# Performance work log

Measured on AMD Instinct MI355X. Metric: run time of the kernel, lower is better.

Reference implementation:

```python
import jax, jax.numpy as jnp
import numpy as np

B, S, I, H = 16, 2048, 1024, 1024


def setup_inputs() -> dict:
    key = jax.random.key(0)
    ks = jax.random.split(key, 12)
    sc = 0.03  # small init so tanh/sigmoid are not saturated
    return {
        "x": jax.random.normal(ks[0], (B, S, I), dtype=jnp.float32),
        "attn_w1": sc * jax.random.normal(ks[1], (H, I), dtype=jnp.float32),
        "attn_b1": sc * jax.random.normal(ks[2], (H,), dtype=jnp.float32),
        "attn_w2": sc * jax.random.normal(ks[3], (1, H), dtype=jnp.float32),
        "attn_b2": sc * jax.random.normal(ks[4], (1,), dtype=jnp.float32),
        "w_ih": sc * jax.random.normal(ks[5], (3 * H, I), dtype=jnp.float32),
        "w_hh": sc * jax.random.normal(ks[6], (3 * H, H), dtype=jnp.float32),
        "b_ih": sc * jax.random.normal(ks[7], (3 * H,), dtype=jnp.float32),
        "b_hh": sc * jax.random.normal(ks[8], (3 * H,), dtype=jnp.float32),
        "fc_w": sc * jax.random.normal(ks[9], (I, H), dtype=jnp.float32),
        "fc_b": sc * jax.random.normal(ks[10], (I,), dtype=jnp.float32),
    }


def reference(x, attn_w1, attn_b1, attn_w2, attn_b2, w_ih, w_hh, b_ih, b_hh, fc_w, fc_b):
    b, s, i = x.shape
    h_dim = w_hh.shape[1]
    # Attention: per-timestep Linear-Tanh-Linear-Softmax, vectorized over time.
    ha = jnp.tanh(jnp.einsum('bsi,hi->bsh', x, attn_w1) + attn_b1)
    scores = jnp.einsum('bsh,oh->bso', ha, attn_w2) + attn_b2  # [B,S,1]
    # torch applies Softmax(dim=1) on [B,1] per timestep -> softmax over size-1 axis
    attn = jax.nn.softmax(scores, axis=2)  # [B,S,1] (identically ones)
    x_w = x * attn
    # GRU (1 layer): precompute input projections over all timesteps.
    gi = jnp.einsum('bsi,gi->bsg', x_w, w_ih) + b_ih  # [B,S,3H]

    def step(h, gi_t):
        gh = h @ w_hh.T + b_hh
        i_r, i_z, i_n = jnp.split(gi_t, 3, axis=-1)
        h_r, h_z, h_n = jnp.split(gh, 3, axis=-1)
        r = jax.nn.sigmoid(i_r + h_r)
        z = jax.nn.sigmoid(i_z + h_z)
        n = jnp.tanh(i_n + r * h_n)
        h_new = (1.0 - z) * n + z * h
        return h_new, h_new

    h0 = jnp.zeros((b, h_dim), dtype=x.dtype)
    h_last, outs = jax.lax.scan(step, h0, jnp.swapaxes(gi, 0, 1))  # outs: [S,B,H]
    rnn_out = jnp.swapaxes(outs, 0, 1)  # [B,S,H]
    output = jnp.einsum('bsh,ih->bsi', rnn_out, fc_w) + fc_b
    hidden = h_last[None]  # [num_layers=1, B, H]
    return (output, hidden, attn)
```

## Files before the change

kernel.cpp:

```cpp
#include <hip/hip_runtime.h>

typedef __attribute__((ext_vector_type(8))) short bh8;
typedef __attribute__((ext_vector_type(4))) float f32x4;

#define BATCH 16
#define SEQ 2048
#define M_ROWS (BATCH * SEQ)
#define KDIM 1024

__device__ __forceinline__ unsigned short f2bf(float f) {
  unsigned u = __float_as_uint(f);
  u = (u + 0x7FFFu + ((u >> 16) & 1u)) >> 16;
  return (unsigned short)u;
}
__device__ __forceinline__ float bf2f(unsigned short h) {
  return __uint_as_float(((unsigned)h) << 16);
}

__device__ __forceinline__ f32x4 mfma_bf16(bh8 a, bh8 b, f32x4 c) {
  return __builtin_amdgcn_mfma_f32_16x16x32_bf16(a, b, c, 0, 0, 0);
}

__device__ __forceinline__ void gl2lds16(const void* g, void* l) {
  __builtin_amdgcn_global_load_lds(
      (const __attribute__((address_space(1))) void*)g,
      (__attribute__((address_space(3))) void*)l, 16, 0, 0);
}

__global__ void cvt_bf16_kernel(const float* __restrict__ in,
                                unsigned short* __restrict__ out, int n4) {
  int i = blockIdx.x * blockDim.x + threadIdx.x;
  if (i >= n4) return;
  float4 v = ((const float4*)in)[i];
  ushort4 o;
  o.x = f2bf(v.x); o.y = f2bf(v.y); o.z = f2bf(v.z); o.w = f2bf(v.w);
  ((ushort4*)out)[i] = o;
}

__global__ void fill_ones_kernel(float* __restrict__ p, int n) {
  int i = blockIdx.x * blockDim.x + threadIdx.x;
  if (i < n) p[i] = 1.0f;
}

template<bool BF16OUT>
__global__ __launch_bounds__(256, 2) void gemm_nt(
    const unsigned short* __restrict__ A,
    const unsigned short* __restrict__ Bm,
    void* __restrict__ Cout,
    const float* __restrict__ bias,
    int N)
{
  __shared__ unsigned short As[128 * 32];
  __shared__ unsigned short Bs[128 * 32];
  const int tid = threadIdx.x;
  const int wave = tid >> 6, lane = tid & 63;
  const long tileM = (long)blockIdx.y * 128;
  const long tileN = (long)blockIdx.x * 128;

  const int srow = wave * 16 + (lane >> 2);
  const int scol = (lane & 3) * 8;
  const unsigned short* ga = A + (tileM + srow) * KDIM + scol;
  const unsigned short* gb = Bm + (tileN + srow) * KDIM + scol;
  unsigned short* la = As + wave * 512;
  unsigned short* lb = Bs + wave * 512;

  f32x4 acc[4][4];
  #pragma unroll
  for (int i = 0; i < 4; ++i)
    #pragma unroll
    for (int j = 0; j < 4; ++j)
      acc[i][j] = (f32x4){0.f, 0.f, 0.f, 0.f};

  const int wm = wave >> 1, wn = wave & 1;
  const int q = lane >> 4, mr = lane & 15;

  #pragma unroll 1
  for (int kt = 0; kt < 32; ++kt) {
    const int ko = kt * 32;
    gl2lds16(ga + ko, la);
    gl2lds16(ga + (long)64 * KDIM + ko, la + 2048);
    gl2lds16(gb + ko, lb);
    gl2lds16(gb + (long)64 * KDIM + ko, lb + 2048);
    __syncthreads();

    bh8 af[4], bfv[4];
    #pragma unroll
    for (int t = 0; t < 4; ++t)
      af[t] = *(const bh8*)&As[(wm * 64 + t * 16 + mr) * 32 + q * 8];
    #pragma unroll
    for (int t = 0; t < 4; ++t)
      bfv[t] = *(const bh8*)&Bs[(wn * 64 + t * 16 + mr) * 32 + q * 8];

    #pragma unroll
    for (int mt = 0; mt < 4; ++mt)
      #pragma unroll
      for (int nt = 0; nt < 4; ++nt)
        acc[mt][nt] = mfma_bf16(af[mt], bfv[nt], acc[mt][nt]);
    __syncthreads();
  }

  #pragma unroll
  for (int mt = 0; mt < 4; ++mt) {
    #pragma unroll
    for (int nt = 0; nt < 4; ++nt) {
      long n = tileN + wn * 64 + nt * 16 + mr;
      #pragma unroll
      for (int i = 0; i < 4; ++i) {
        long m = tileM + wm * 64 + mt * 16 + q * 4 + i;
        if constexpr (BF16OUT) {
          ((unsigned short*)Cout)[m * N + n] = f2bf(acc[mt][nt][i]);
        } else {
          ((float*)Cout)[m * N + n] = acc[mt][nt][i] + bias[n];
        }
      }
    }
  }
}

#define GRU_WGS 64
__global__ __launch_bounds__(256, 1) void gru_kernel(
    const unsigned short* __restrict__ gi,
    const unsigned short* __restrict__ whh,
    const float* __restrict__ b_ih,
    const float* __restrict__ b_hh,
    unsigned short* __restrict__ hbuf,
    unsigned short* __restrict__ rnn,
    float* __restrict__ hidden_out,
    unsigned* __restrict__ ctr)
{
  const int wg = blockIdx.x;
  const int tid = threadIdx.x;
  const int wv = tid >> 6, lane = tid & 63;
  const int D0 = wg * 16;
  const int q = lane >> 4, nn = lane & 15;

  bh8 wf[3][8];
  #pragma unroll
  for (int g = 0; g < 3; ++g)
    #pragma unroll
    for (int kk = 0; kk < 8; ++kk) {
      int k = wv * 256 + kk * 32 + q * 8;
      wf[g][kk] = *(const bh8*)&whh[(size_t)(g * 1024 + D0 + nn) * 1024 + k];
    }

  const int b = tid >> 4, dd = tid & 15, d = D0 + dd;
  const float bir = b_ih[d], biz = b_ih[1024 + d], bin_ = b_ih[2048 + d];
  const float bhr = b_hh[d], bhz = b_hh[1024 + d], bhn = b_hh[2048 + d];
  float hreg = 0.0f;
  const unsigned short* gi_base = gi + (size_t)b * SEQ * 3072 + d;

  __shared__ float red[4][3][16][16];

  #pragma unroll 1
  for (int s = 0; s < SEQ; ++s) {
    const unsigned short* hsrc = hbuf + (s & 1) * 16384;
    unsigned short* hdst = hbuf + ((s + 1) & 1) * 16384;

    f32x4 acc0 = {0.f,0.f,0.f,0.f}, acc1 = {0.f,0.f,0.f,0.f}, acc2 = {0.f,0.f,0.f,0.f};
    #pragma unroll
    for (int kk = 0; kk < 8; ++kk) {
      int k = wv * 256 + kk * 32 + q * 8;
      bh8 af = *(const bh8*)&hsrc[nn * 1024 + k];
      acc0 = mfma_bf16(af, wf[0][kk], acc0);
      acc1 = mfma_bf16(af, wf[1][kk], acc1);
      acc2 = mfma_bf16(af, wf[2][kk], acc2);
    }
    #pragma unroll
    for (int i = 0; i < 4; ++i) {
      red[wv][0][q * 4 + i][nn] = acc0[i];
      red[wv][1][q * 4 + i][nn] = acc1[i];
      red[wv][2][q * 4 + i][nn] = acc2[i];
    }
    __syncthreads();

    float ghr = red[0][0][b][dd] + red[1][0][b][dd] + red[2][0][b][dd] + red[3][0][b][dd];
    float ghz = red[0][1][b][dd] + red[1][1][b][dd] + red[2][1][b][dd] + red[3][1][b][dd];
    float ghn = red[0][2][b][dd] + red[1][2][b][dd] + red[2][2][b][dd] + red[3][2][b][dd];

    const unsigned short* gr = gi_base + (size_t)s * 3072;
    float gir = bf2f(gr[0]);
    float giz = bf2f(gr[1024]);
    float gin = bf2f(gr[2048]);

    float xr = gir + bir + ghr + bhr;
    float xz = giz + biz + ghz + bhz;
    float r = 1.0f / (1.0f + __expf(-xr));
    float z = 1.0f / (1.0f + __expf(-xz));
    float u = gin + bin_ + r * (ghn + bhn);
    float e = __expf(-2.0f * fabsf(u));
    float t = (1.0f - e) / (1.0f + e);
    float nv = copysignf(t, u);
    hreg = (1.0f - z) * nv + z * hreg;

    unsigned short hb = f2bf(hreg);
    hdst[b * 1024 + d] = hb;
    rnn[((size_t)b * SEQ + s) * 1024 + d] = hb;
    if (s == SEQ - 1) hidden_out[b * 1024 + d] = hreg;

    __syncthreads();
    if (tid == 0) {
      __hip_atomic_fetch_add(&ctr[s], 1u, __ATOMIC_RELEASE, __HIP_MEMORY_SCOPE_AGENT);
      unsigned v;
      do {
        v = __hip_atomic_load(&ctr[s], __ATOMIC_RELAXED, __HIP_MEMORY_SCOPE_AGENT);
      } while (v < (unsigned)GRU_WGS);
      (void)__hip_atomic_load(&ctr[s], __ATOMIC_ACQUIRE, __HIP_MEMORY_SCOPE_AGENT);
    }
    __syncthreads();
  }
}

extern "C" void kernel_launch(void* const* d_in, const int* in_sizes, int n_in,
                              void* d_out, int out_size, void* d_ws, size_t ws_size,
                              hipStream_t stream) {
  const float* x    = (const float*)d_in[0];
  const float* w_ih = (const float*)d_in[5];
  const float* w_hh = (const float*)d_in[6];
  const float* b_ih = (const float*)d_in[7];
  const float* b_hh = (const float*)d_in[8];
  const float* fc_w = (const float*)d_in[9];
  const float* fc_b = (const float*)d_in[10];

  float* out        = (float*)d_out;
  float* hidden_out = out + (size_t)M_ROWS * 1024;
  float* attn_out   = hidden_out + 16 * 1024;

  char* ws = (char*)d_ws;
  unsigned short* x_bf   = (unsigned short*)(ws);
  unsigned short* wih_bf = (unsigned short*)(ws + 67108864);
  unsigned short* whh_bf = (unsigned short*)(ws + 73400320);
  unsigned short* fcw_bf = (unsigned short*)(ws + 79691776);
  unsigned short* gi_bf  = (unsigned short*)(ws + 81788928);
  unsigned short* rnn_bf = (unsigned short*)(ws + 283115520);
  unsigned short* hbuf   = (unsigned short*)(ws + 350224384);
  unsigned*       ctr    = (unsigned*)(ws + 350289920);

  hipMemsetAsync(hbuf, 0, 65536 + 8192, stream);

  cvt_bf16_kernel<<<32768, 256, 0, stream>>>(x, x_bf, 8388608);
  cvt_bf16_kernel<<<3072, 256, 0, stream>>>(w_ih, wih_bf, 786432);
  cvt_bf16_kernel<<<3072, 256, 0, stream>>>(w_hh, whh_bf, 786432);
  cvt_bf16_kernel<<<1024, 256, 0, stream>>>(fc_w, fcw_bf, 262144);
  fill_ones_kernel<<<128, 256, 0, stream>>>(attn_out, 32768);

  gemm_nt<true><<<dim3(24, 256), 256, 0, stream>>>(x_bf, wih_bf, gi_bf, nullptr, 3072);

  gru_kernel<<<GRU_WGS, 256, 0, stream>>>(gi_bf, whh_bf, b_ih, b_hh, hbuf, rnn_bf,
                                          hidden_out, ctr);

  gemm_nt<false><<<dim3(8, 256), 256, 0, stream>>>(rnn_bf, fcw_bf, out, fc_b, 1024);
}
```

Baseline: 13.39 ms.

## Replace GRU grid barrier with step-tagged hidden-state words and polled loads

```diff
diff --git a/kernel.cpp b/kernel.cpp
--- a/kernel.cpp
+++ b/kernel.cpp
@@ -42,7 +42,7 @@
   if (i < n) p[i] = 1.0f;
 }
 
-template<bool BF16OUT>
+template<int MODE>
 __global__ __launch_bounds__(256, 2) void gemm_nt(
     const unsigned short* __restrict__ A,
     const unsigned short* __restrict__ Bm,
@@ -107,10 +107,13 @@
       #pragma unroll
       for (int i = 0; i < 4; ++i) {
         long m = tileM + wm * 64 + mt * 16 + q * 4 + i;
-        if constexpr (BF16OUT) {
-          ((unsigned short*)Cout)[m * N + n] = f2bf(acc[mt][nt][i]);
+        if constexpr (MODE == 0) {
+          ((float*)Cout)[m * N + n] = acc[mt][nt][i] + bias[n];
         } else {
-          ((float*)Cout)[m * N + n] = acc[mt][nt][i] + bias[n];
+          int b = (int)(m >> 11), s = (int)(m & 2047);
+          int g = (int)(n >> 10), wgi = (int)((n >> 4) & 63), dd = (int)(n & 15);
+          size_t idx = ((size_t)s * 64 + wgi) * 768 + (size_t)g * 256 + b * 16 + dd;
+          ((unsigned short*)Cout)[idx] = f2bf(acc[mt][nt][i]);
         }
       }
     }
@@ -123,10 +126,9 @@
     const unsigned short* __restrict__ whh,
     const float* __restrict__ b_ih,
     const float* __restrict__ b_hh,
-    unsigned short* __restrict__ hbuf,
+    unsigned* __restrict__ hdw,
     unsigned short* __restrict__ rnn,
-    float* __restrict__ hidden_out,
-    unsigned* __restrict__ ctr)
+    float* __restrict__ hidden_out)
 {
   const int wg = blockIdx.x;
   const int tid = threadIdx.x;
@@ -147,23 +149,43 @@
   const float bir = b_ih[d], biz = b_ih[1024 + d], bin_ = b_ih[2048 + d];
   const float bhr = b_hh[d], bhz = b_hh[1024 + d], bhn = b_hh[2048 + d];
   float hreg = 0.0f;
-  const unsigned short* gi_base = gi + (size_t)b * SEQ * 3072 + d;
 
   __shared__ float red[4][3][16][16];
 
   #pragma unroll 1
   for (int s = 0; s < SEQ; ++s) {
-    const unsigned short* hsrc = hbuf + (s & 1) * 16384;
-    unsigned short* hdst = hbuf + ((s + 1) & 1) * 16384;
+    const unsigned short* gbase = gi + ((size_t)s * 64 + wg) * 768 + b * 16 + dd;
+    float gir = bf2f(gbase[0]);
+    float giz = bf2f(gbase[256]);
+    float gin = bf2f(gbase[512]);
+
+    const unsigned* hrow = hdw + (s & 1) * 16384 + nn * 1024 + wv * 256 + q * 8;
+    unsigned t[64];
+    const unsigned tgtw = (unsigned)s << 16;
+    for (;;) {
+      #pragma unroll
+      for (int kk = 0; kk < 8; ++kk)
+        #pragma unroll
+        for (int e = 0; e < 8; ++e)
+          t[kk * 8 + e] = __hip_atomic_load(&hrow[kk * 32 + e], __ATOMIC_RELAXED,
+                                            __HIP_MEMORY_SCOPE_AGENT);
+      unsigned bad = 0;
+      #pragma unroll
+      for (int i = 0; i < 64; ++i) bad |= (t[i] ^ tgtw);
+      if ((bad & 0xffff0000u) == 0u) break;
+    }
 
     f32x4 acc0 = {0.f,0.f,0.f,0.f}, acc1 = {0.f,0.f,0.f,0.f}, acc2 = {0.f,0.f,0.f,0.f};
     #pragma unroll
     for (int kk = 0; kk < 8; ++kk) {
-      int k = wv * 256 + kk * 32 + q * 8;
-      bh8 af = *(const bh8*)&hsrc[nn * 1024 + k];
-      acc0 = mfma_bf16(af, wf[0][kk], acc0);
-      acc1 = mfma_bf16(af, wf[1][kk], acc1);
-      acc2 = mfma_bf16(af, wf[2][kk], acc2);
+      union { unsigned w[4]; bh8 v; } u;
+      u.w[0] = __builtin_amdgcn_perm(t[kk*8+1], t[kk*8+0], 0x05040100u);
+      u.w[1] = __builtin_amdgcn_perm(t[kk*8+3], t[kk*8+2], 0x05040100u);
+      u.w[2] = __builtin_amdgcn_perm(t[kk*8+5], t[kk*8+4], 0x05040100u);
+      u.w[3] = __builtin_amdgcn_perm(t[kk*8+7], t[kk*8+6], 0x05040100u);
+      acc0 = mfma_bf16(u.v, wf[0][kk], acc0);
+      acc1 = mfma_bf16(u.v, wf[1][kk], acc1);
+      acc2 = mfma_bf16(u.v, wf[2][kk], acc2);
     }
     #pragma unroll
     for (int i = 0; i < 4; ++i) {
@@ -177,35 +199,24 @@
     float ghz = red[0][1][b][dd] + red[1][1][b][dd] + red[2][1][b][dd] + red[3][1][b][dd];
     float ghn = red[0][2][b][dd] + red[1][2][b][dd] + red[2][2][b][dd] + red[3][2][b][dd];
 
-    const unsigned short* gr = gi_base + (size_t)s * 3072;
-    float gir = bf2f(gr[0]);
-    float giz = bf2f(gr[1024]);
-    float gin = bf2f(gr[2048]);
-
     float xr = gir + bir + ghr + bhr;
     float xz = giz + biz + ghz + bhz;
     float r = 1.0f / (1.0f + __expf(-xr));
     float z = 1.0f / (1.0f + __expf(-xz));
-    float u = gin + bin_ + r * (ghn + bhn);
-    float e = __expf(-2.0f * fabsf(u));
-    float t = (1.0f - e) / (1.0f + e);
-    float nv = copysignf(t, u);
+    float u_ = gin + bin_ + r * (ghn + bhn);
+    float e = __expf(-2.0f * fabsf(u_));
+    float tt = (1.0f - e) / (1.0f + e);
+    float nv = copysignf(tt, u_);
     hreg = (1.0f - z) * nv + z * hreg;
 
     unsigned short hb = f2bf(hreg);
-    hdst[b * 1024 + d] = hb;
+    __hip_atomic_store(&hdw[((s + 1) & 1) * 16384 + b * 1024 + d],
+                       (((unsigned)(s + 1)) << 16) | (unsigned)hb,
+                       __ATOMIC_RELAXED, __HIP_MEMORY_SCOPE_AGENT);
+
     rnn[((size_t)b * SEQ + s) * 1024 + d] = hb;
     if (s == SEQ - 1) hidden_out[b * 1024 + d] = hreg;
 
-    __syncthreads();
-    if (tid == 0) {
-      __hip_atomic_fetch_add(&ctr[s], 1u, __ATOMIC_RELEASE, __HIP_MEMORY_SCOPE_AGENT);
-      unsigned v;
-      do {
-        v = __hip_atomic_load(&ctr[s], __ATOMIC_RELAXED, __HIP_MEMORY_SCOPE_AGENT);
-      } while (v < (unsigned)GRU_WGS);
-      (void)__hip_atomic_load(&ctr[s], __ATOMIC_ACQUIRE, __HIP_MEMORY_SCOPE_AGENT);
-    }
     __syncthreads();
   }
 }
@@ -232,10 +243,9 @@
   unsigned short* fcw_bf = (unsigned short*)(ws + 79691776);
   unsigned short* gi_bf  = (unsigned short*)(ws + 81788928);
   unsigned short* rnn_bf = (unsigned short*)(ws + 283115520);
-  unsigned short* hbuf   = (unsigned short*)(ws + 350224384);
-  unsigned*       ctr    = (unsigned*)(ws + 350289920);
-
-  hipMemsetAsync(hbuf, 0, 65536 + 8192, stream);
+  unsigned*       hdw    = (unsigned*)(ws + 350224384);
+
+  hipMemsetAsync(hdw, 0, 131072, stream);
 
   cvt_bf16_kernel<<<32768, 256, 0, stream>>>(x, x_bf, 8388608);
   cvt_bf16_kernel<<<3072, 256, 0, stream>>>(w_ih, wih_bf, 786432);
@@ -243,10 +253,10 @@
   cvt_bf16_kernel<<<1024, 256, 0, stream>>>(fc_w, fcw_bf, 262144);
   fill_ones_kernel<<<128, 256, 0, stream>>>(attn_out, 32768);
 
-  gemm_nt<true><<<dim3(24, 256), 256, 0, stream>>>(x_bf, wih_bf, gi_bf, nullptr, 3072);
-
-  gru_kernel<<<GRU_WGS, 256, 0, stream>>>(gi_bf, whh_bf, b_ih, b_hh, hbuf, rnn_bf,
-                                          hidden_out, ctr);
-
-  gemm_nt<false><<<dim3(8, 256), 256, 0, stream>>>(rnn_bf, fcw_bf, out, fc_b, 1024);
-}
+  gemm_nt<2><<<dim3(24, 256), 256, 0, stream>>>(x_bf, wih_bf, gi_bf, nullptr, 3072);
+
+  gru_kernel<<<GRU_WGS, 256, 0, stream>>>(gi_bf, whh_bf, b_ih, b_hh, hdw, rnn_bf,
+                                          hidden_out);
+
+  gemm_nt<0><<<dim3(8, 256), 256, 0, stream>>>(rnn_bf, fcw_bf, out, fc_b, 1024);
+}
```

After: 23.95 ms. 1.79x slower.
